# Kernel tuning notes

Hardware: AMD Instinct MI355X
Metric: run time of the kernel (lower is better)

## Reference

```python
import jax, jax.numpy as jnp
import numpy as np

B, C, H, W = 512, 2048, 8, 8   # batch, backbone channels, feature-map HxW (cfg.output_hm_shape)
J = 30                          # smpl.pos_joint_num
CF = 512                        # conv output channels
EPS = 1e-5                      # BatchNorm eps


def setup_inputs() -> dict:
    key = jax.random.key(0)
    ks = jax.random.split(key, 10)
    D = J * (CF + 3)  # 15450
    return {
        "img_feat": jax.random.normal(ks[0], (B, C, H, W), jnp.float32),
        # joint coords in heatmap pixel space [0, W-1] (x, y, z)
        "joint_coord_img": jax.random.uniform(ks[1], (B, J, 3), jnp.float32) * (W - 1),
        "conv_w": jax.random.normal(ks[2], (CF, C), jnp.float32) * 0.02,
        "conv_b": jnp.zeros((CF,), jnp.float32),
        "bn_gamma": jnp.ones((CF,), jnp.float32),
        "bn_beta": jnp.zeros((CF,), jnp.float32),
        "bn_mean": jnp.zeros((CF,), jnp.float32),
        "bn_var": jnp.ones((CF,), jnp.float32),
        "root_w": jax.random.normal(ks[3], (6, D), jnp.float32) * 0.01,
        "root_b": jnp.zeros((6,), jnp.float32),
        "pose_w": jax.random.normal(ks[4], (126, D), jnp.float32) * 0.01,
        "pose_b": jnp.zeros((126,), jnp.float32),
        "shape_w": jax.random.normal(ks[5], (10, C), jnp.float32) * 0.01,
        "shape_b": jnp.zeros((10,), jnp.float32),
        "cam_w": jax.random.normal(ks[6], (3, C), jnp.float32) * 0.01,
        "cam_b": jnp.zeros((3,), jnp.float32),
    }


def _bilinear_sample(feat, xy):
    """Batched bilinear sample == F.grid_sample(align_corners=True, padding='zeros')
    with grid built directly from pixel coords in [0, W-1].
    feat: (B, Cf, H, W), xy: (B, J, 2) pixel coords -> (B, J, Cf)."""
    x, y = xy[..., 0], xy[..., 1]
    x0f, y0f = jnp.floor(x), jnp.floor(y)
    wx1, wy1 = x - x0f, y - y0f
    wx0, wy0 = 1.0 - wx1, 1.0 - wy1
    x0, y0 = x0f.astype(jnp.int32), y0f.astype(jnp.int32)
    x1, y1 = x0 + 1, y0 + 1

    def corner(yi, xi, wt):
        valid = (xi >= 0) & (xi < feat.shape[3]) & (yi >= 0) & (yi < feat.shape[2])
        yc = jnp.clip(yi, 0, feat.shape[2] - 1)
        xc = jnp.clip(xi, 0, feat.shape[3] - 1)
        # gather (B, Cf, J) via vmap over batch
        g = jax.vmap(lambda f, yy, xx: f[:, yy, xx])(feat, yc, xc)
        return g * (wt * valid.astype(feat.dtype))[:, None, :]

    out = (corner(y0, x0, wy0 * wx0) + corner(y0, x1, wy0 * wx1)
           + corner(y1, x0, wy1 * wx0) + corner(y1, x1, wy1 * wx1))
    return jnp.transpose(out, (0, 2, 1))  # (B, J, Cf)


def reference(img_feat, joint_coord_img, conv_w, conv_b, bn_gamma, bn_beta,
              bn_mean, bn_var, root_w, root_b, pose_w, pose_b,
              shape_w, shape_b, cam_w, cam_b):
    bsz = img_feat.shape[0]
    pooled = img_feat.mean(axis=(2, 3))                       # (B, 2048)
    shape_param = pooled @ shape_w.T + shape_b                # (B, 10)
    cam_param = pooled @ cam_w.T + cam_b                      # (B, 3)

    # 1x1 conv + BatchNorm (eval) + ReLU
    f = jnp.einsum('bchw,oc->bohw', img_feat, conv_w) + conv_b[None, :, None, None]
    f = (f - bn_mean[None, :, None, None]) * jax.lax.rsqrt(bn_var + EPS)[None, :, None, None]
    f = jax.nn.relu(f * bn_gamma[None, :, None, None] + bn_beta[None, :, None, None])

    # fused per-joint bilinear gather (replaces the per-joint python loop)
    img_feat_joints = _bilinear_sample(f, joint_coord_img[..., :2])  # (B, J, 512)
    feat = jnp.concatenate([img_feat_joints, joint_coord_img], axis=2)  # (B, J, 515)
    feat = feat.reshape(bsz, -1)                              # (B, 15450)

    root_pose = feat @ root_w.T + root_b                      # (B, 6)
    pose_param = feat @ pose_w.T + pose_b                     # (B, 126)
    return (root_pose, pose_param, shape_param, cam_param)
```

## Files before the change

kernel.cpp:

```cpp
#include <hip/hip_runtime.h>
#include <stdint.h>

typedef __attribute__((ext_vector_type(8))) short bf16x8;
typedef __attribute__((ext_vector_type(4))) float f32x4;

__device__ __forceinline__ unsigned short f2bf(float f) {
    union { float f; uint32_t u; } v; v.f = f;
    uint32_t r = (v.u + 0x7FFFu + ((v.u >> 16) & 1u)) >> 16;
    return (unsigned short)r;
}
__device__ __forceinline__ float bf2f(unsigned short u) {
    union { uint32_t u; float f; } v; v.u = ((uint32_t)u) << 16; return v.f;
}

__device__ __forceinline__ void gload16(const void* g, void* l) {
    __builtin_amdgcn_global_load_lds(
        (const __attribute__((address_space(1))) unsigned int*)g,
        (__attribute__((address_space(3))) unsigned int*)l, 16, 0, 0);
}

#define WP_ELEMS  1081344
#define K2        15456
#define W2P_ELEMS (144 * K2)

#define ABUF0  0
#define ABUF1  33792
#define BBUF0  67584
#define BBUF1  71680
#define REDOFF 75776
#define SMEM_SZ 76032

#define WAIT_VM8 asm volatile("s_waitcnt vmcnt(8) lgkmcnt(0)" ::: "memory")
#define WAIT_VM0 asm volatile("s_waitcnt vmcnt(0) lgkmcnt(0)" ::: "memory")
#define BAR do { __builtin_amdgcn_s_barrier(); __builtin_amdgcn_sched_barrier(0); } while (0)

__global__ void prep_kernel(const float* __restrict__ cw,
                            const float* __restrict__ sw,
                            const float* __restrict__ camw,
                            const float* __restrict__ root_w,
                            const float* __restrict__ pose_w,
                            const float* __restrict__ cb, const float* __restrict__ g,
                            const float* __restrict__ be, const float* __restrict__ m,
                            const float* __restrict__ vv,
                            unsigned short* __restrict__ Wp,
                            unsigned short* __restrict__ W2p,
                            float* __restrict__ sbws) {
    int gid = blockIdx.x * 256 + threadIdx.x;
    if (gid < WP_ELEMS) {
        int kt  = gid / 16896;
        int rem = gid - kt * 16896;
        int gg  = rem >> 9;
        int r2  = rem & 511;
        int q   = r2 >> 7;
        int rr  = (r2 >> 3) & 15;
        int e   = r2 & 7;
        int row = gg * 16 + rr;
        int k   = kt * 32 + q * 8 + e;
        float v = 0.f;
        if (row < 512)      v = cw[row * 2048 + k];
        else if (row < 522) v = sw[(row - 512) * 2048 + k];
        else if (row < 525) v = camw[(row - 522) * 2048 + k];
        Wp[gid] = f2bf(v);
        return;
    }
    gid -= WP_ELEMS;
    if (gid < W2P_ELEMS) {
        int o2 = gid / K2;
        int kk = gid - o2 * K2;
        float v = 0.f;
        if (o2 < 132) {
            const float* wr = (o2 < 6) ? (root_w + o2 * 15450) : (pose_w + (o2 - 6) * 15450);
            if (kk < 15360) {
                int j = kk >> 9;
                int o = kk & 511;
                v = wr[j * 515 + o];
            } else {
                int c = kk - 15360;
                if (c < 90) {
                    int j = c / 3, d = c - 3 * j;
                    v = wr[j * 515 + 512 + d];
                }
            }
        }
        W2p[gid] = f2bf(v);
        return;
    }
    gid -= W2P_ELEMS;
    if (gid < 512) {
        float s = g[gid] * rsqrtf(vv[gid] + 1e-5f);
        sbws[2 * gid]     = s;
        sbws[2 * gid + 1] = be[gid] + s * (cb[gid] - m[gid]);
    }
}

__global__ __launch_bounds__(256, 2)
void conv_main_kernel(const float* __restrict__ img,
                      const float* __restrict__ jc,
                      const unsigned short* __restrict__ Wp,
                      const float* __restrict__ sbws,
                      const float* __restrict__ shape_b,
                      const float* __restrict__ cam_b,
                      unsigned short* __restrict__ sampled,
                      float* __restrict__ out) {
    __shared__ __align__(16) char smem[SMEM_SZ];
    const int t    = threadIdx.x;
    const int lane = t & 63;
    const int w    = t >> 6;
    const int l15  = lane & 15;
    const int quad = lane >> 4;
    const int b    = blockIdx.x;

    f32x4 acc[8][4];
    f32x4 accX;
    #pragma unroll
    for (int mi = 0; mi < 8; ++mi)
        #pragma unroll
        for (int nt = 0; nt < 4; ++nt)
            acc[mi][nt] = (f32x4){0.f, 0.f, 0.f, 0.f};
    accX = (f32x4){0.f, 0.f, 0.f, 0.f};

    const float* gBbase = img + (size_t)b * 131072 + (size_t)(w * 8) * 64 + lane;
    float fbA[8], fbB[8];

    auto loadB = [&](int kt, float* fb) {
        const float* gB = gBbase + (size_t)(kt * 32) * 64;
        #pragma unroll
        for (int j = 0; j < 8; ++j) fb[j] = gB[j * 64];
    };
    auto writeB = [&](const float* fb, char* bbuf) {
        int4 bv;
        bv.x = (int)((uint32_t)f2bf(fb[0]) | ((uint32_t)f2bf(fb[1]) << 16));
        bv.y = (int)((uint32_t)f2bf(fb[2]) | ((uint32_t)f2bf(fb[3]) << 16));
        bv.z = (int)((uint32_t)f2bf(fb[4]) | ((uint32_t)f2bf(fb[5]) << 16));
        bv.w = (int)((uint32_t)f2bf(fb[6]) | ((uint32_t)f2bf(fb[7]) << 16));
        *(int4*)(bbuf + (lane >> 4) * 1024 + w * 256 + l15 * 16) = bv;
    };
    auto stageA = [&](int kt, char* abuf) {
        const unsigned short* base = Wp + (size_t)kt * 16896;
        const unsigned short* src  = base + (size_t)(w * 8) * 512 + lane * 8;
        char* dst = abuf + w * 8192;
        #pragma unroll
        for (int i = 0; i < 8; ++i)
            gload16(src + i * 512, dst + i * 1024);
        gload16(base + 32 * 512 + lane * 8, abuf + 32768);
    };
    auto compute = [&](const char* abuf, const char* bbuf) {
        bf16x8 bfr0 = *(const bf16x8*)(bbuf + 0 * 1024 + quad * 256 + l15 * 16);
        bf16x8 bfr1 = *(const bf16x8*)(bbuf + 1 * 1024 + quad * 256 + l15 * 16);
        bf16x8 bfr2 = *(const bf16x8*)(bbuf + 2 * 1024 + quad * 256 + l15 * 16);
        bf16x8 bfr3 = *(const bf16x8*)(bbuf + 3 * 1024 + quad * 256 + l15 * 16);
        #pragma unroll
        for (int mi = 0; mi < 8; ++mi) {
            bf16x8 afr = *(const bf16x8*)(abuf + (w * 8 + mi) * 1024 + quad * 256 + l15 * 16);
            acc[mi][0] = __builtin_amdgcn_mfma_f32_16x16x32_bf16(afr, bfr0, acc[mi][0], 0, 0, 0);
            acc[mi][1] = __builtin_amdgcn_mfma_f32_16x16x32_bf16(afr, bfr1, acc[mi][1], 0, 0, 0);
            acc[mi][2] = __builtin_amdgcn_mfma_f32_16x16x32_bf16(afr, bfr2, acc[mi][2], 0, 0, 0);
            acc[mi][3] = __builtin_amdgcn_mfma_f32_16x16x32_bf16(afr, bfr3, acc[mi][3], 0, 0, 0);
        }
        {
            bf16x8 afrX = *(const bf16x8*)(abuf + 32768 + quad * 256 + l15 * 16);
            bf16x8 bfrW = *(const bf16x8*)(bbuf + w * 1024 + quad * 256 + l15 * 16);
            accX = __builtin_amdgcn_mfma_f32_16x16x32_bf16(afrX, bfrW, accX, 0, 0, 0);
        }
    };

    loadB(0, fbA);
    stageA(0, smem + ABUF0);
    loadB(1, fbB);
    writeB(fbA, smem + BBUF0);
    WAIT_VM8;
    BAR;

    #pragma unroll 1
    for (int kt = 0; kt < 64; kt += 2) {
        {
            if (kt < 63) stageA(kt + 1, smem + ABUF1);
            if (kt < 62) loadB(kt + 2, fbA);
            compute(smem + ABUF0, smem + BBUF0);
            if (kt < 63) writeB(fbB, smem + BBUF1);
            if (kt < 62) { WAIT_VM8; } else { WAIT_VM0; }
            BAR;
        }
        {
            int k1 = kt + 1;
            if (k1 < 63) stageA(k1 + 1, smem + ABUF0);
            if (k1 < 62) loadB(k1 + 2, fbB);
            compute(smem + ABUF1, smem + BBUF1);
            if (k1 < 63) writeB(fbA, smem + BBUF0);
            if (k1 < 62) { WAIT_VM8; } else { WAIT_VM0; }
            BAR;
        }
    }

    __syncthreads();
    const float2* sb2 = (const float2*)sbws;
    #pragma unroll
    for (int mi = 0; mi < 8; ++mi) {
        #pragma unroll
        for (int r = 0; r < 4; ++r) {
            int row = w * 128 + mi * 16 + quad * 4 + r;
            float2 sb = sb2[row];
            #pragma unroll
            for (int nt = 0; nt < 4; ++nt) {
                int col = nt * 16 + l15;
                float v = fmaxf(acc[mi][nt][r] * sb.x + sb.y, 0.f);
                *(unsigned short*)(smem + row * 128 + (((col + row) & 63) << 1)) = f2bf(v);
            }
        }
    }
    float* red = (float*)(smem + REDOFF);
    #pragma unroll
    for (int r = 0; r < 4; ++r) {
        float v = accX[r];
        v += __shfl_xor(v, 1);
        v += __shfl_xor(v, 2);
        v += __shfl_xor(v, 4);
        v += __shfl_xor(v, 8);
        if (l15 == 0) red[w * 16 + quad * 4 + r] = v;
    }
    __syncthreads();

    if (t < 16) {
        float v = (red[t] + red[16 + t] + red[32 + t] + red[48 + t]) * 0.015625f;
        if (t < 10)      out[67584 + b * 10 + t] = v + shape_b[t];
        else if (t < 13) out[72704 + b * 3 + (t - 10)] = v + cam_b[t - 10];
    }
    const float* jcb = jc + b * 90;
    if (t < 96) {
        float v = (t < 90) ? jcb[t] : 0.f;
        sampled[(size_t)b * K2 + 15360 + t] = f2bf(v);
    }

    unsigned int* outsamp = (unsigned int*)(sampled + (size_t)b * K2);
    const int o = 2 * t;
    for (int s = 0; s < 30; ++s) {
        float x = jcb[s * 3 + 0];
        float y = jcb[s * 3 + 1];
        float x0f = floorf(x), y0f = floorf(y);
        int x0 = (int)x0f, y0 = (int)y0f;
        int x1 = x0 + 1, y1 = y0 + 1;
        float wx1 = x - x0f, wy1 = y - y0f;
        float wx0 = 1.f - wx1, wy0 = 1.f - wy1;
        float vx0 = (x0 >= 0 && x0 < 8) ? 1.f : 0.f;
        float vx1 = (x1 >= 0 && x1 < 8) ? 1.f : 0.f;
        float vy0 = (y0 >= 0 && y0 < 8) ? 1.f : 0.f;
        float vy1 = (y1 >= 0 && y1 < 8) ? 1.f : 0.f;
        int cx0 = min(max(x0, 0), 7), cx1 = min(max(x1, 0), 7);
        int cy0 = min(max(y0, 0), 7), cy1 = min(max(y1, 0), 7);
        int p00 = cy0 * 8 + cx0, p01 = cy0 * 8 + cx1;
        int p10 = cy1 * 8 + cx0, p11 = cy1 * 8 + cx1;
        float w00 = wy0 * wx0 * vy0 * vx0, w01 = wy0 * wx1 * vy0 * vx1;
        float w10 = wy1 * wx0 * vy1 * vx0, w11 = wy1 * wx1 * vy1 * vx1;
        float vA = w00 * bf2f(*(unsigned short*)(smem + o * 128 + (((p00 + o) & 63) << 1)))
                 + w01 * bf2f(*(unsigned short*)(smem + o * 128 + (((p01 + o) & 63) << 1)))
                 + w10 * bf2f(*(unsigned short*)(smem + o * 128 + (((p10 + o) & 63) << 1)))
                 + w11 * bf2f(*(unsigned short*)(smem + o * 128 + (((p11 + o) & 63) << 1)));
        int o1 = o + 1;
        float vB = w00 * bf2f(*(unsigned short*)(smem + o1 * 128 + (((p00 + o1) & 63) << 1)))
                 + w01 * bf2f(*(unsigned short*)(smem + o1 * 128 + (((p01 + o1) & 63) << 1)))
                 + w10 * bf2f(*(unsigned short*)(smem + o1 * 128 + (((p10 + o1) & 63) << 1)))
                 + w11 * bf2f(*(unsigned short*)(smem + o1 * 128 + (((p11 + o1) & 63) << 1)));
        outsamp[s * 256 + t] = (uint32_t)f2bf(vA) | ((uint32_t)f2bf(vB) << 16);
    }
}

__global__ __launch_bounds__(256, 4)
void gemm2_kernel(const unsigned short* __restrict__ sampled,
                  const unsigned short* __restrict__ W2p,
                  float* __restrict__ part) {
    __shared__ __align__(16) char smem[16640];
    const int t    = threadIdx.x;
    const int lane = t & 63;
    const int w    = t >> 6;
    const int l15  = lane & 15;
    const int quad = lane >> 4;
    const int m0   = blockIdx.x * 64;
    const int j    = blockIdx.y;
    const int k0   = j * 512;
    const int ktn  = (j == 30) ? 3 : 16;

    f32x4 acc[9];
    #pragma unroll
    for (int nt = 0; nt < 9; ++nt) acc[nt] = (f32x4){0.f, 0.f, 0.f, 0.f};

    for (int kt = 0; kt < ktn; ++kt) {
        __syncthreads();
        {
            int r = t >> 2, ci = t & 3;
            int4 d = *(const int4*)(sampled + (size_t)(m0 + r) * K2 + k0 + kt * 32 + ci * 8);
            *(int4*)(smem + r * 80 + ci * 16) = d;
        }
        #pragma unroll
        for (int i = 0; i < 3; ++i) {
            int c2 = t + 256 * i;
            if (c2 < 576) {
                int r = c2 >> 2, ci = c2 & 3;
                int4 d = *(const int4*)(W2p + (size_t)r * K2 + k0 + kt * 32 + ci * 8);
                *(int4*)(smem + 5120 + r * 80 + ci * 16) = d;
            }
        }
        __syncthreads();
        bf16x8 a = *(const bf16x8*)(smem + (w * 16 + l15) * 80 + quad * 16);
        #pragma unroll
        for (int nt = 0; nt < 9; ++nt) {
            bf16x8 bfv = *(const bf16x8*)(smem + 5120 + (nt * 16 + l15) * 80 + quad * 16);
            acc[nt] = __builtin_amdgcn_mfma_f32_16x16x32_bf16(a, bfv, acc[nt], 0, 0, 0);
        }
    }
    float* pout = part + (size_t)(j * 8 + blockIdx.x) * 9216;
    #pragma unroll
    for (int nt = 0; nt < 9; ++nt) {
        #pragma unroll
        for (int r = 0; r < 4; ++r) {
            pout[(w * 16 + quad * 4 + r) * 144 + nt * 16 + l15] = acc[nt][r];
        }
    }
}

__global__ void reduce_out_kernel(const float* __restrict__ part,
                                  const float* __restrict__ root_b,
                                  const float* __restrict__ pose_b,
                                  float* __restrict__ out) {
    int gid = blockIdx.x * 256 + threadIdx.x;
    int m  = gid / 132;
    int o2 = gid - m * 132;
    float s = (o2 < 6) ? root_b[o2] : pose_b[o2 - 6];
    const float* p = part + (size_t)(m >> 6) * 9216 + (m & 63) * 144 + o2;
    #pragma unroll
    for (int j = 0; j < 31; ++j) s += p[(size_t)j * 8 * 9216];
    if (o2 < 6) out[m * 6 + o2] = s;
    else        out[3072 + m * 126 + (o2 - 6)] = s;
}

extern "C" void kernel_launch(void* const* d_in, const int* in_sizes, int n_in,
                              void* d_out, int out_size, void* d_ws, size_t ws_size,
                              hipStream_t stream) {
    const float* img     = (const float*)d_in[0];
    const float* jc      = (const float*)d_in[1];
    const float* conv_w  = (const float*)d_in[2];
    const float* conv_b  = (const float*)d_in[3];
    const float* bn_g    = (const float*)d_in[4];
    const float* bn_be   = (const float*)d_in[5];
    const float* bn_m    = (const float*)d_in[6];
    const float* bn_v    = (const float*)d_in[7];
    const float* root_w  = (const float*)d_in[8];
    const float* root_b  = (const float*)d_in[9];
    const float* pose_w  = (const float*)d_in[10];
    const float* pose_b  = (const float*)d_in[11];
    const float* shape_w = (const float*)d_in[12];
    const float* shape_b = (const float*)d_in[13];
    const float* cam_w   = (const float*)d_in[14];
    const float* cam_b   = (const float*)d_in[15];
    float* out = (float*)d_out;
    char* ws = (char*)d_ws;

    unsigned short* Wp   = (unsigned short*)(ws);
    unsigned short* W2p  = (unsigned short*)(ws + 2162688);
    unsigned short* samp = (unsigned short*)(ws + 6614016);
    float* part          = (float*)(ws + 22440960);
    float* sbws          = (float*)(ws + 31583232);

    prep_kernel<<<12920, 256, 0, stream>>>(conv_w, shape_w, cam_w, root_w, pose_w,
                                           conv_b, bn_g, bn_be, bn_m, bn_v,
                                           Wp, W2p, sbws);
    conv_main_kernel<<<512, 256, 0, stream>>>(img, jc, Wp, sbws, shape_b, cam_b,
                                              samp, out);
    gemm2_kernel<<<dim3(8, 31), 256, 0, stream>>>(samp, W2p, part);
    reduce_out_kernel<<<264, 256, 0, stream>>>(part, root_b, pose_b, out);
}
```

Measured before the change: 464.2 us.

## Load conv weight fragments directly into registers instead of staging through LDS

The conv GEMM main loop no longer stages the per-k-tile weight block into shared memory with global_load_lds. Each wave now loads its A fragments straight from global memory into registers, one tile ahead, and B fragments are read with inline-asm ds_read_b128 using precomputed LDS addresses. This cuts LDS traffic and shrinks shared memory, but it adds register pressure (nine bf16x8 prefetch registers) and exposes global-load latency inside the loop. The reworked waitcnt discipline also relies on the compiler inserting vmcnt waits before the registers are used.

```diff
diff --git a/kernel.cpp b/kernel.cpp
--- a/kernel.cpp
+++ b/kernel.cpp
@@ -12,27 +12,18 @@
 __device__ __forceinline__ float bf2f(unsigned short u) {
     union { uint32_t u; float f; } v; v.u = ((uint32_t)u) << 16; return v.f;
 }
-
-__device__ __forceinline__ void gload16(const void* g, void* l) {
-    __builtin_amdgcn_global_load_lds(
-        (const __attribute__((address_space(1))) unsigned int*)g,
-        (__attribute__((address_space(3))) unsigned int*)l, 16, 0, 0);
+__device__ __forceinline__ unsigned lds_addr(const void* p) {
+    return (unsigned)(size_t)(const __attribute__((address_space(3))) char*)p;
 }
 
 #define WP_ELEMS  1081344
 #define K2        15456
 #define W2P_ELEMS (144 * K2)
 
-#define ABUF0  0
-#define ABUF1  33792
-#define BBUF0  67584
-#define BBUF1  71680
-#define REDOFF 75776
-#define SMEM_SZ 76032
-
-#define WAIT_VM8 asm volatile("s_waitcnt vmcnt(8) lgkmcnt(0)" ::: "memory")
-#define WAIT_VM0 asm volatile("s_waitcnt vmcnt(0) lgkmcnt(0)" ::: "memory")
 #define BAR do { __builtin_amdgcn_s_barrier(); __builtin_amdgcn_sched_barrier(0); } while (0)
+#define LGKM0 asm volatile("s_waitcnt lgkmcnt(0)" ::: "memory")
+#define DSR(d, a)      asm volatile("ds_read_b128 %0, %1"           : "=v"(d) : "v"(a))
+#define DSRO(d, a, o)  asm volatile("ds_read_b128 %0, %1 offset:" o : "=v"(d) : "v"(a))
 
 __global__ void prep_kernel(const float* __restrict__ cw,
                             const float* __restrict__ sw,
@@ -102,7 +93,7 @@
                       const float* __restrict__ cam_b,
                       unsigned short* __restrict__ sampled,
                       float* __restrict__ out) {
-    __shared__ __align__(16) char smem[SMEM_SZ];
+    __shared__ __align__(16) char smem[65536 + 256];
     const int t    = threadIdx.x;
     const int lane = t & 63;
     const int w    = t >> 6;
@@ -135,60 +126,79 @@
         bv.w = (int)((uint32_t)f2bf(fb[6]) | ((uint32_t)f2bf(fb[7]) << 16));
         *(int4*)(bbuf + (lane >> 4) * 1024 + w * 256 + l15 * 16) = bv;
     };
-    auto stageA = [&](int kt, char* abuf) {
-        const unsigned short* base = Wp + (size_t)kt * 16896;
-        const unsigned short* src  = base + (size_t)(w * 8) * 512 + lane * 8;
-        char* dst = abuf + w * 8192;
-        #pragma unroll
-        for (int i = 0; i < 8; ++i)
-            gload16(src + i * 512, dst + i * 1024);
-        gload16(base + 32 * 512 + lane * 8, abuf + 32768);
+    const unsigned short* aSrc = Wp + (size_t)(w * 4096) + quad * 128 + l15 * 8;
+    const unsigned short* xSrc = Wp + 16384 + quad * 128 + l15 * 8;
+    bf16x8 aa[8], ax;
+    auto loadA = [&](int kt) {
+        const unsigned short* s = aSrc + (size_t)kt * 16896;
+        #pragma unroll
+        for (int i = 0; i < 8; ++i) aa[i] = *(const bf16x8*)(s + i * 512);
+        ax = *(const bf16x8*)(xSrc + (size_t)kt * 16896);
     };
-    auto compute = [&](const char* abuf, const char* bbuf) {
-        bf16x8 bfr0 = *(const bf16x8*)(bbuf + 0 * 1024 + quad * 256 + l15 * 16);
-        bf16x8 bfr1 = *(const bf16x8*)(bbuf + 1 * 1024 + quad * 256 + l15 * 16);
-        bf16x8 bfr2 = *(const bf16x8*)(bbuf + 2 * 1024 + quad * 256 + l15 * 16);
-        bf16x8 bfr3 = *(const bf16x8*)(bbuf + 3 * 1024 + quad * 256 + l15 * 16);
-        #pragma unroll
-        for (int mi = 0; mi < 8; ++mi) {
-            bf16x8 afr = *(const bf16x8*)(abuf + (w * 8 + mi) * 1024 + quad * 256 + l15 * 16);
-            acc[mi][0] = __builtin_amdgcn_mfma_f32_16x16x32_bf16(afr, bfr0, acc[mi][0], 0, 0, 0);
-            acc[mi][1] = __builtin_amdgcn_mfma_f32_16x16x32_bf16(afr, bfr1, acc[mi][1], 0, 0, 0);
-            acc[mi][2] = __builtin_amdgcn_mfma_f32_16x16x32_bf16(afr, bfr2, acc[mi][2], 0, 0, 0);
-            acc[mi][3] = __builtin_amdgcn_mfma_f32_16x16x32_bf16(afr, bfr3, acc[mi][3], 0, 0, 0);
-        }
-        {
-            bf16x8 afrX = *(const bf16x8*)(abuf + 32768 + quad * 256 + l15 * 16);
-            bf16x8 bfrW = *(const bf16x8*)(bbuf + w * 1024 + quad * 256 + l15 * 16);
-            accX = __builtin_amdgcn_mfma_f32_16x16x32_bf16(afrX, bfrW, accX, 0, 0, 0);
-        }
-    };
-
+
+    const unsigned fo    = (unsigned)(quad * 256 + l15 * 16);
+    const unsigned adrB0 = lds_addr(smem) + fo;
+    const unsigned adrB1 = lds_addr(smem) + 4096 + fo;
+    const unsigned adrW0 = lds_addr(smem) + (unsigned)(w * 1024) + fo;
+    const unsigned adrW1 = lds_addr(smem) + 4096 + (unsigned)(w * 1024) + fo;
+
+    loadA(0);
     loadB(0, fbA);
-    stageA(0, smem + ABUF0);
     loadB(1, fbB);
-    writeB(fbA, smem + BBUF0);
-    WAIT_VM8;
+    writeB(fbA, smem);
+    LGKM0;
     BAR;
 
     #pragma unroll 1
     for (int kt = 0; kt < 64; kt += 2) {
         {
-            if (kt < 63) stageA(kt + 1, smem + ABUF1);
+            bf16x8 bb0, bb1, bb2, bb3, bw;
+            DSR (bb0, adrB0);
+            DSRO(bb1, adrB0, "1024");
+            DSRO(bb2, adrB0, "2048");
+            DSRO(bb3, adrB0, "3072");
+            DSR (bw, adrW0);
             if (kt < 62) loadB(kt + 2, fbA);
-            compute(smem + ABUF0, smem + BBUF0);
-            if (kt < 63) writeB(fbB, smem + BBUF1);
-            if (kt < 62) { WAIT_VM8; } else { WAIT_VM0; }
+            LGKM0;
+            __builtin_amdgcn_sched_barrier(0);
+            #pragma unroll
+            for (int mi = 0; mi < 8; ++mi) {
+                acc[mi][0] = __builtin_amdgcn_mfma_f32_16x16x32_bf16(aa[mi], bb0, acc[mi][0], 0, 0, 0);
+                acc[mi][1] = __builtin_amdgcn_mfma_f32_16x16x32_bf16(aa[mi], bb1, acc[mi][1], 0, 0, 0);
+                acc[mi][2] = __builtin_amdgcn_mfma_f32_16x16x32_bf16(aa[mi], bb2, acc[mi][2], 0, 0, 0);
+                acc[mi][3] = __builtin_amdgcn_mfma_f32_16x16x32_bf16(aa[mi], bb3, acc[mi][3], 0, 0, 0);
+            }
+            accX = __builtin_amdgcn_mfma_f32_16x16x32_bf16(ax, bw, accX, 0, 0, 0);
+            loadA(kt + 1);
+            writeB(fbB, smem + 4096);
+            LGKM0;
             BAR;
         }
         {
-            int k1 = kt + 1;
-            if (k1 < 63) stageA(k1 + 1, smem + ABUF0);
+            const int k1 = kt + 1;
+            bf16x8 bb0, bb1, bb2, bb3, bw;
+            DSR (bb0, adrB1);
+            DSRO(bb1, adrB1, "1024");
+            DSRO(bb2, adrB1, "2048");
+            DSRO(bb3, adrB1, "3072");
+            DSR (bw, adrW1);
             if (k1 < 62) loadB(k1 + 2, fbB);
-            compute(smem + ABUF1, smem + BBUF1);
-            if (k1 < 63) writeB(fbA, smem + BBUF0);
-            if (k1 < 62) { WAIT_VM8; } else { WAIT_VM0; }
-            BAR;
+            LGKM0;
+            __builtin_amdgcn_sched_barrier(0);
+            #pragma unroll
+            for (int mi = 0; mi < 8; ++mi) {
+                acc[mi][0] = __builtin_amdgcn_mfma_f32_16x16x32_bf16(aa[mi], bb0, acc[mi][0], 0, 0, 0);
+                acc[mi][1] = __builtin_amdgcn_mfma_f32_16x16x32_bf16(aa[mi], bb1, acc[mi][1], 0, 0, 0);
+                acc[mi][2] = __builtin_amdgcn_mfma_f32_16x16x32_bf16(aa[mi], bb2, acc[mi][2], 0, 0, 0);
+                acc[mi][3] = __builtin_amdgcn_mfma_f32_16x16x32_bf16(aa[mi], bb3, acc[mi][3], 0, 0, 0);
+            }
+            accX = __builtin_amdgcn_mfma_f32_16x16x32_bf16(ax, bw, accX, 0, 0, 0);
+            if (k1 < 63) {
+                loadA(k1 + 1);
+                writeB(fbA, smem);
+                LGKM0;
+                BAR;
+            }
         }
     }
 
@@ -208,7 +218,7 @@
             }
         }
     }
-    float* red = (float*)(smem + REDOFF);
+    float* red = (float*)(smem + 65536);
     #pragma unroll
     for (int r = 0; r < 4; ++r) {
         float v = accX[r];
```

New measurement: 467.0 us. About the same (+0.6%).
